# Performance work log

Hardware: AMD Instinct MI355X
Metric: run time of the kernel (lower is better)

## Reference

```python
import jax, jax.numpy as jnp
import numpy as np

IMG = 416                      # image_shape
DIST = 1075.0                  # isocenter_distance
N_ANG = 320                    # 360 / rotation_resolution(=1.125 deg)
N_DET = IMG                    # detector bins
N_SAMP = IMG                   # integration samples per ray
SCALE = 512.0 / 416.0 * 0.03   # self.scale


def _ray_coords():
    """Pixel-space sample coordinates for every (angle, detector, sample).
    Returns cols, rows of shape [N_ANG, N_DET, N_SAMP] and the step length dt."""
    thetas = (jnp.arange(N_ANG, dtype=jnp.float32) * np.float32(2.0 * np.pi / N_ANG))
    half_diag = (IMG / 2.0) * np.sqrt(2.0)
    gamma_max = np.float32(np.arcsin(half_diag / DIST))  # half fan angle covering image
    gammas = jnp.linspace(-gamma_max, gamma_max, N_DET, dtype=jnp.float32)
    ray_len = np.float32(IMG * np.sqrt(2.0))             # chord length through image
    ts = jnp.linspace(np.float32(DIST - ray_len / 2.0),
                      np.float32(DIST + ray_len / 2.0), N_SAMP, dtype=jnp.float32)
    dt = float(ray_len / (N_SAMP - 1))

    th = thetas[:, None, None]        # [A,1,1]
    gm = gammas[None, :, None]        # [1,D,1]
    t = ts[None, None, :]             # [1,1,S]
    # source position on circle of radius DIST, ray direction toward detector
    sx = np.float32(DIST) * jnp.cos(th)
    sy = np.float32(DIST) * jnp.sin(th)
    x = sx - t * jnp.cos(th + gm)     # [A,D,S] world coords (isocenter at origin)
    y = sy - t * jnp.sin(th + gm)
    ctr = np.float32((IMG - 1) / 2.0)
    return x + ctr, y + ctr, dt       # pixel (col, row) coordinates


def _bilinear(img, cols, rows):
    """Zero-padded bilinear sampling of img[H,W] at float (row,col) coords."""
    c0 = jnp.floor(cols)
    r0 = jnp.floor(rows)
    wc = cols - c0
    wr = rows - r0
    c0i = c0.astype(jnp.int32)
    r0i = r0.astype(jnp.int32)

    def g(ri, ci):
        inb = (ri >= 0) & (ri < IMG) & (ci >= 0) & (ci < IMG)
        v = img[jnp.clip(ri, 0, IMG - 1), jnp.clip(ci, 0, IMG - 1)]
        return jnp.where(inb, v, jnp.float32(0.0))

    return (g(r0i, c0i) * (1 - wr) * (1 - wc)
            + g(r0i, c0i + 1) * (1 - wr) * wc
            + g(r0i + 1, c0i) * wr * (1 - wc)
            + g(r0i + 1, c0i + 1) * wr * wc)


def fan_beam_fp(vol):
    """vol: [B,H,W] -> sinogram [B, N_ANG, N_DET] via ray integration."""
    cols, rows, dt = _ray_coords()
    proj_one = lambda img: _bilinear(img, cols, rows).sum(axis=-1) * jnp.float32(dt)
    return jax.vmap(proj_one)(vol)


def setup_inputs() -> dict:
    key = jax.random.key(0)
    k1, k2 = jax.random.split(key)
    inp = jax.random.normal(k1, (1, 1, IMG, IMG), dtype=jnp.float32)
    tgt = jax.random.normal(k2, (1, 1, IMG, IMG), dtype=jnp.float32)
    return {"input": inp, "target": tgt}


def reference(input, target):
    input_proj = fan_beam_fp(input[:, 0])   # squeeze(1)
    target_proj = fan_beam_fp(target[:, 0])
    return jnp.mean((input_proj - target_proj) ** 2) * jnp.float32(SCALE)
```

## Files before the change

kernel.cpp:

```cpp
#include <hip/hip_runtime.h>
#include <math.h>

#define IMG 416
#define N_ANG 320
#define N_DET 416
#define N_SAMP 416

#define GSTRIDE 464
#define GROWS   432
#define GBYTES  ((size_t)GROWS * GSTRIDE)
#define GWORDS  (GROWS * GSTRIDE / 4)

#define SPLANE  (N_ANG * N_DET)
#define SBYTES  ((size_t)4 * SPLANE * sizeof(float))
#define WSNEED  (GBYTES + SBYTES)

#define LROWS   228
#define LSTRIDE 232

typedef float vfloat2 __attribute__((ext_vector_type(2)));

__global__ __launch_bounds__(256) void pack_kernel(const float* __restrict__ a,
                                                   const float* __restrict__ b,
                                                   unsigned int* __restrict__ G,
                                                   float* __restrict__ out) {
    int i = blockIdx.x * 256 + threadIdx.x;
    if (i == 0) out[0] = 0.0f;
    if (i >= GWORDS) return;
    int pr = i / (GSTRIDE / 4);
    int wc = i - pr * (GSTRIDE / 4);
    int r  = pr - 8;
    int c0 = wc * 4 - 8;
    float v[4];
    #pragma unroll
    for (int j = 0; j < 4; ++j) {
        int c = c0 + j;
        float val = 0.0f;
        if ((unsigned)r < (unsigned)IMG && (unsigned)c < (unsigned)IMG) {
            int idx = r * IMG + c;
            val = a[idx] - b[idx];
        }
        v[j] = val;
    }
    unsigned int u = __builtin_amdgcn_cvt_pk_fp8_f32(v[0], v[1], 0u, false);
    u = __builtin_amdgcn_cvt_pk_fp8_f32(v[2], v[3], u, true);
    G[i] = u;
}

__global__ void zero_out_kernel(float* __restrict__ out) {
    if (threadIdx.x == 0) out[0] = 0.0f;
}

__global__ __launch_bounds__(448) void proj_lds(const unsigned int* __restrict__ G,
                                                float* __restrict__ S,
                                                float theta_step, float gmax,
                                                float gstep, float t0,
                                                float dtstep) {
    __shared__ unsigned char L[LROWS * LSTRIDE];

    const int blk = blockIdx.x;
    const int a  = blk >> 2;
    const int q  = blk & 3;
    const int qi = q >> 1, qj = q & 1;
    const int r0 = qi ? 222 : -2;
    const int c0 = qj ? 220 : -4;
    const int nrows = qi ? 197 : 227;

    {
        const int gbase = ((r0 + 8) * GSTRIDE + (c0 + 8)) >> 2;
        const int total = nrows * 58;
        for (int i = threadIdx.x; i < total; i += 448) {
            int rr = i / 58;
            int cc = i - rr * 58;
            unsigned int w = G[gbase + rr * 116 + cc];
            *(unsigned int*)(&L[rr * LSTRIDE + cc * 4]) = w;
        }
    }
    __syncthreads();

    const int d = threadIdx.x;
    if (d < N_DET) {
        const float theta = (float)a * theta_step;
        const float gamma = fmaf((float)d, gstep, -gmax);
        float s1, c1, s2, c2;
        sincosf(theta, &s1, &c1);
        sincosf(theta + gamma, &s2, &c2);
        const float sx = fmaf(1075.0f, c1, 207.5f);
        const float sy = fmaf(1075.0f, s1, 207.5f);

        const float C0 = fmaf(-t0, c2, sx), dc = dtstep * c2;
        const float R0 = fmaf(-t0, s2, sy), dr = dtstep * s2;

        const float cl = qj ? 224.0f : -2.0f, ch = qj ? 418.0f : 224.0f;
        const float rl = qi ? 224.0f : -2.0f, rh = qi ? 418.0f : 224.0f;

        int klo = 0, khi = N_SAMP - 1;
        auto clip1 = [&](float X0, float dX, float lo, float hi) {
            if (fabsf(dX) < 1e-8f) {
                if (!(X0 >= lo && X0 < hi)) { klo = 1; khi = 0; }
            } else {
                float x1 = (X0 - hi) / dX;
                float x2 = (X0 - lo) / dX;
                x1 = fminf(fmaxf(x1, -1e6f), 1e6f);
                x2 = fminf(fmaxf(x2, -1e6f), 1e6f);
                int lo_k, hi_k;
                if (dX > 0.0f) { lo_k = (int)floorf(x1) + 1; hi_k = (int)floorf(x2); }
                else           { lo_k = (int)ceilf(x2);      hi_k = (int)ceilf(x1) - 1; }
                klo = max(klo, lo_k);
                khi = min(khi, hi_k);
            }
        };
        clip1(C0, dc, cl, ch);
        clip1(R0, dr, rl, rh);

        float acc = 0.0f;
        if (klo <= khi) {
            float colR = fmaf(-(float)klo, dc, C0) - (float)c0;
            float rowR = fmaf(-(float)klo, dr, R0) - (float)r0;
            #pragma unroll 4
            for (int k = klo; k <= khi; ++k) {
                const int ci = (int)colR;
                const int ri = (int)rowR;
                const float wc = colR - (float)ci;
                const float wr = rowR - (float)ri;
                const int base = ri * LSTRIDE + ci;
                const unsigned int b00 = L[base];
                const unsigned int b01 = L[base + 1];
                const unsigned int b10 = L[base + LSTRIDE];
                const unsigned int b11 = L[base + LSTRIDE + 1];
                const vfloat2 lo2 = __builtin_amdgcn_cvt_pk_f32_fp8(b00 | (b01 << 8), false);
                const vfloat2 hi2 = __builtin_amdgcn_cvt_pk_f32_fp8(b10 | (b11 << 8), false);
                const float top = fmaf(wc, lo2[1] - lo2[0], lo2[0]);
                const float bot = fmaf(wc, hi2[1] - hi2[0], hi2[0]);
                acc = fmaf(wr, bot - top, acc + top);
                colR -= dc;
                rowR -= dr;
            }
        }
        S[q * SPLANE + a * N_DET + d] = acc;
    }
}

__global__ __launch_bounds__(256) void reduce_kernel(const float* __restrict__ S,
                                                     float* __restrict__ out,
                                                     float coef) {
    const int i = blockIdx.x * 256 + threadIdx.x;
    float v = 0.0f;
    if (i < SPLANE)
        v = (S[i] + S[SPLANE + i]) + (S[2 * SPLANE + i] + S[3 * SPLANE + i]);
    float sq = v * v;
    #pragma unroll
    for (int m = 32; m > 0; m >>= 1) sq += __shfl_down(sq, m, 64);
    __shared__ float w[4];
    const int lane = threadIdx.x & 63;
    if (lane == 0) w[threadIdx.x >> 6] = sq;
    __syncthreads();
    if (threadIdx.x == 0)
        atomicAdd(out, (w[0] + w[1] + w[2] + w[3]) * coef);
}

__global__ __launch_bounds__(256) void proj_fused(const float* __restrict__ imgA,
                                                  const float* __restrict__ imgB,
                                                  float* __restrict__ out,
                                                  float theta_step, float gmax,
                                                  float gstep, float t0,
                                                  float dtstep, float coef) {
    const int idx = blockIdx.x * 256 + threadIdx.x;
    const int a  = idx / N_DET;
    const int dd = idx - a * N_DET;
    const float theta = (float)a * theta_step;
    const float gamma = fmaf((float)dd, gstep, -gmax);
    float s1, c1, s2, c2;
    sincosf(theta, &s1, &c1);
    sincosf(theta + gamma, &s2, &c2);
    const float sx = 1075.0f * c1 + 207.5f;
    const float sy = 1075.0f * s1 + 207.5f;
    float acc = 0.0f;
    #pragma unroll 4
    for (int s = 0; s < N_SAMP; ++s) {
        const float t   = fmaf((float)s, dtstep, t0);
        const float col = fmaf(-t, c2, sx);
        const float row = fmaf(-t, s2, sy);
        const float c0 = floorf(col);
        const float r0 = floorf(row);
        const float wc = col - c0;
        const float wr = row - r0;
        const int ci = (int)c0;
        const int ri = (int)r0;
        auto Gv = [&](int r, int c) -> float {
            if ((unsigned)r < (unsigned)IMG && (unsigned)c < (unsigned)IMG)
                return imgA[r * IMG + c] - imgB[r * IMG + c];
            return 0.0f;
        };
        const float v00 = Gv(ri, ci);
        const float v01 = Gv(ri, ci + 1);
        const float v10 = Gv(ri + 1, ci);
        const float v11 = Gv(ri + 1, ci + 1);
        const float top = fmaf(wc, v01 - v00, v00);
        const float bot = fmaf(wc, v11 - v10, v10);
        acc += fmaf(wr, bot - top, top);
    }
    float sq = acc * acc;
    #pragma unroll
    for (int o = 32; o > 0; o >>= 1) sq += __shfl_down(sq, o, 64);
    __shared__ float wsum[4];
    const int lane = threadIdx.x & 63;
    if (lane == 0) wsum[threadIdx.x >> 6] = sq;
    __syncthreads();
    if (threadIdx.x == 0)
        atomicAdd(out, (wsum[0] + wsum[1] + wsum[2] + wsum[3]) * coef);
}

extern "C" void kernel_launch(void* const* d_in, const int* in_sizes, int n_in,
                              void* d_out, int out_size, void* d_ws, size_t ws_size,
                              hipStream_t stream) {
    const float* in = (const float*)d_in[0];
    const float* tg = (const float*)d_in[1];
    float* out = (float*)d_out;

    const double half_diag = (IMG / 2.0) * sqrt(2.0);
    const double ray_len   = IMG * sqrt(2.0);
    const float  gmax      = (float)asin(half_diag / 1075.0);
    const float  gstep     = (float)(2.0 * (double)gmax / (N_DET - 1));
    const float  t0        = (float)(1075.0 - ray_len / 2.0);
    const float  dtstep    = (float)(ray_len / (N_SAMP - 1));
    const float  theta_step = (float)(2.0 * M_PI / N_ANG);
    const double dt        = ray_len / (N_SAMP - 1);
    const double SCALE     = 512.0 / 416.0 * 0.03;
    const float  coef      = (float)(dt * dt * SCALE / ((double)N_ANG * N_DET));

    if (ws_size >= WSNEED) {
        unsigned int* G = (unsigned int*)d_ws;
        float* S = (float*)((char*)d_ws + GBYTES);
        pack_kernel<<<(GWORDS + 255) / 256, 256, 0, stream>>>(in, tg, G, out);
        proj_lds<<<N_ANG * 4, 448, 0, stream>>>(G, S, theta_step, gmax, gstep,
                                                t0, dtstep);
        reduce_kernel<<<SPLANE / 256, 256, 0, stream>>>(S, out, coef);
    } else {
        zero_out_kernel<<<1, 64, 0, stream>>>(out);
        proj_fused<<<(N_ANG * N_DET) / 256, 256, 0, stream>>>(
            in, tg, out, theta_step, gmax, gstep, t0, dtstep, coef);
    }
}
```

Measured before the change: 105.5 us.

## Pack 2x2 fp8 quads per word, split image into 16 tiles, atomic-accumulate

The packed difference image now stores each pixel's 2x2 bilinear neighbourhood as four fp8 bytes in one 32-bit word, so each sample needs one LDS load instead of four byte loads. The image is split into a 4x4 grid of 104-pixel tiles per angle (16 blocks per angle instead of 4), which shrinks the LDS footprint and raises parallelism; tiles are loaded with 16-byte vector copies. Partial ray sums are combined with atomicAdd into a single sinogram plane zeroed by the pack kernel, removing the 4-plane reduction. This costs 4x global storage for the packed image, more redundant tile loads and more per-block setup per ray, plus float atomics with nondeterministic summation order.

```diff
diff --git a/kernel.cpp b/kernel.cpp
--- a/kernel.cpp
+++ b/kernel.cpp
@@ -6,74 +6,71 @@
 #define N_DET 416
 #define N_SAMP 416
 
-#define GSTRIDE 464
-#define GROWS   432
-#define GBYTES  ((size_t)GROWS * GSTRIDE)
-#define GWORDS  (GROWS * GSTRIDE / 4)
+#define GQSTRIDE 424
+#define GQROWS   420
+#define GQWORDS  (GQROWS * GQSTRIDE)
+#define GQBYTES  ((size_t)GQWORDS * 4)
 
 #define SPLANE  (N_ANG * N_DET)
-#define SBYTES  ((size_t)4 * SPLANE * sizeof(float))
-#define WSNEED  (GBYTES + SBYTES)
-
-#define LROWS   228
-#define LSTRIDE 232
+#define SBYTES  ((size_t)SPLANE * 4)
+#define WSNEED  (GQBYTES + SBYTES)
+
+#define LSTRIDE 116
+#define LWORDS  (108 * LSTRIDE)
 
 typedef float vfloat2 __attribute__((ext_vector_type(2)));
 
 __global__ __launch_bounds__(256) void pack_kernel(const float* __restrict__ a,
                                                    const float* __restrict__ b,
-                                                   unsigned int* __restrict__ G,
+                                                   unsigned int* __restrict__ Gq,
+                                                   float* __restrict__ S,
                                                    float* __restrict__ out) {
     int i = blockIdx.x * 256 + threadIdx.x;
     if (i == 0) out[0] = 0.0f;
-    if (i >= GWORDS) return;
-    int pr = i / (GSTRIDE / 4);
-    int wc = i - pr * (GSTRIDE / 4);
-    int r  = pr - 8;
-    int c0 = wc * 4 - 8;
-    float v[4];
-    #pragma unroll
-    for (int j = 0; j < 4; ++j) {
-        int c = c0 + j;
-        float val = 0.0f;
+    if (i < SPLANE) S[i] = 0.0f;
+    if (i >= GQWORDS) return;
+    int row  = i / GQSTRIDE;
+    int colw = i - row * GQSTRIDE;
+    int pr = row - 2, pc = colw - 2;
+    auto D = [&](int r, int c) -> float {
         if ((unsigned)r < (unsigned)IMG && (unsigned)c < (unsigned)IMG) {
             int idx = r * IMG + c;
-            val = a[idx] - b[idx];
+            return a[idx] - b[idx];
         }
-        v[j] = val;
-    }
-    unsigned int u = __builtin_amdgcn_cvt_pk_fp8_f32(v[0], v[1], 0u, false);
-    u = __builtin_amdgcn_cvt_pk_fp8_f32(v[2], v[3], u, true);
-    G[i] = u;
+        return 0.0f;
+    };
+    const float v00 = D(pr, pc),     v01 = D(pr, pc + 1);
+    const float v10 = D(pr + 1, pc), v11 = D(pr + 1, pc + 1);
+    unsigned int u = __builtin_amdgcn_cvt_pk_fp8_f32(v00, v01, 0u, false);
+    u = __builtin_amdgcn_cvt_pk_fp8_f32(v10, v11, u, true);
+    Gq[i] = u;
 }
 
 __global__ void zero_out_kernel(float* __restrict__ out) {
     if (threadIdx.x == 0) out[0] = 0.0f;
 }
 
-__global__ __launch_bounds__(448) void proj_lds(const unsigned int* __restrict__ G,
+__global__ __launch_bounds__(448) void proj_lds(const unsigned int* __restrict__ Gq,
                                                 float* __restrict__ S,
                                                 float theta_step, float gmax,
                                                 float gstep, float t0,
                                                 float dtstep) {
-    __shared__ unsigned char L[LROWS * LSTRIDE];
-
-    const int blk = blockIdx.x;
-    const int a  = blk >> 2;
-    const int q  = blk & 3;
-    const int qi = q >> 1, qj = q & 1;
-    const int r0 = qi ? 222 : -2;
-    const int c0 = qj ? 220 : -4;
-    const int nrows = qi ? 197 : 227;
+    __shared__ unsigned int Lw[LWORDS];
+
+    const int blk  = blockIdx.x;
+    const int a    = blk >> 4;
+    const int tile = blk & 15;
+    const int qi = tile >> 2, qj = tile & 3;
+    const int r0 = 104 * qi - 2;
+    const int c0 = 104 * qj - 2;
 
     {
-        const int gbase = ((r0 + 8) * GSTRIDE + (c0 + 8)) >> 2;
-        const int total = nrows * 58;
-        for (int i = threadIdx.x; i < total; i += 448) {
-            int rr = i / 58;
-            int cc = i - rr * 58;
-            unsigned int w = G[gbase + rr * 116 + cc];
-            *(unsigned int*)(&L[rr * LSTRIDE + cc * 4]) = w;
+        const uint4* __restrict__ src =
+            (const uint4*)(Gq + (r0 + 2) * GQSTRIDE + (c0 + 2));
+        for (int i = threadIdx.x; i < 108 * 27; i += 448) {
+            int rr = i / 27, cc = i - rr * 27;
+            uint4 w = src[rr * (GQSTRIDE / 4) + cc];
+            *(uint4*)&Lw[rr * LSTRIDE + cc * 4] = w;
         }
     }
     __syncthreads();
@@ -91,16 +88,19 @@
         const float C0 = fmaf(-t0, c2, sx), dc = dtstep * c2;
         const float R0 = fmaf(-t0, s2, sy), dr = dtstep * s2;
 
-        const float cl = qj ? 224.0f : -2.0f, ch = qj ? 418.0f : 224.0f;
-        const float rl = qi ? 224.0f : -2.0f, rh = qi ? 418.0f : 224.0f;
+        const float cl = (qj == 0) ? -1.0f : 104.0f * qj;
+        const float ch = (qj == 3) ? 416.0f : 104.0f * (qj + 1);
+        const float rl = (qi == 0) ? -1.0f : 104.0f * qi;
+        const float rh = (qi == 3) ? 416.0f : 104.0f * (qi + 1);
 
         int klo = 0, khi = N_SAMP - 1;
         auto clip1 = [&](float X0, float dX, float lo, float hi) {
             if (fabsf(dX) < 1e-8f) {
                 if (!(X0 >= lo && X0 < hi)) { klo = 1; khi = 0; }
             } else {
-                float x1 = (X0 - hi) / dX;
-                float x2 = (X0 - lo) / dX;
+                const float inv = 1.0f / dX;
+                float x1 = (X0 - hi) * inv;
+                float x2 = (X0 - lo) * inv;
                 x1 = fminf(fmaxf(x1, -1e6f), 1e6f);
                 x2 = fminf(fmaxf(x2, -1e6f), 1e6f);
                 int lo_k, hi_k;
@@ -113,31 +113,27 @@
         clip1(C0, dc, cl, ch);
         clip1(R0, dr, rl, rh);
 
-        float acc = 0.0f;
         if (klo <= khi) {
             float colR = fmaf(-(float)klo, dc, C0) - (float)c0;
             float rowR = fmaf(-(float)klo, dr, R0) - (float)r0;
+            float acc = 0.0f;
             #pragma unroll 4
             for (int k = klo; k <= khi; ++k) {
                 const int ci = (int)colR;
                 const int ri = (int)rowR;
                 const float wc = colR - (float)ci;
                 const float wr = rowR - (float)ri;
-                const int base = ri * LSTRIDE + ci;
-                const unsigned int b00 = L[base];
-                const unsigned int b01 = L[base + 1];
-                const unsigned int b10 = L[base + LSTRIDE];
-                const unsigned int b11 = L[base + LSTRIDE + 1];
-                const vfloat2 lo2 = __builtin_amdgcn_cvt_pk_f32_fp8(b00 | (b01 << 8), false);
-                const vfloat2 hi2 = __builtin_amdgcn_cvt_pk_f32_fp8(b10 | (b11 << 8), false);
+                const unsigned int u = Lw[ri * LSTRIDE + ci];
+                const vfloat2 lo2 = __builtin_amdgcn_cvt_pk_f32_fp8(u, false);
+                const vfloat2 hi2 = __builtin_amdgcn_cvt_pk_f32_fp8(u, true);
                 const float top = fmaf(wc, lo2[1] - lo2[0], lo2[0]);
                 const float bot = fmaf(wc, hi2[1] - hi2[0], hi2[0]);
                 acc = fmaf(wr, bot - top, acc + top);
                 colR -= dc;
                 rowR -= dr;
             }
+            atomicAdd(&S[a * N_DET + d], acc);
         }
-        S[q * SPLANE + a * N_DET + d] = acc;
     }
 }
 
@@ -145,9 +141,7 @@
                                                      float* __restrict__ out,
                                                      float coef) {
     const int i = blockIdx.x * 256 + threadIdx.x;
-    float v = 0.0f;
-    if (i < SPLANE)
-        v = (S[i] + S[SPLANE + i]) + (S[2 * SPLANE + i] + S[3 * SPLANE + i]);
+    float v = (i < SPLANE) ? S[i] : 0.0f;
     float sq = v * v;
     #pragma unroll
     for (int m = 32; m > 0; m >>= 1) sq += __shfl_down(sq, m, 64);
@@ -230,12 +224,12 @@
     const float  coef      = (float)(dt * dt * SCALE / ((double)N_ANG * N_DET));
 
     if (ws_size >= WSNEED) {
-        unsigned int* G = (unsigned int*)d_ws;
-        float* S = (float*)((char*)d_ws + GBYTES);
-        pack_kernel<<<(GWORDS + 255) / 256, 256, 0, stream>>>(in, tg, G, out);
-        proj_lds<<<N_ANG * 4, 448, 0, stream>>>(G, S, theta_step, gmax, gstep,
-                                                t0, dtstep);
-        reduce_kernel<<<SPLANE / 256, 256, 0, stream>>>(S, out, coef);
+        unsigned int* Gq = (unsigned int*)d_ws;
+        float* S = (float*)((char*)d_ws + GQBYTES);
+        pack_kernel<<<(GQWORDS + 255) / 256, 256, 0, stream>>>(in, tg, Gq, S, out);
+        proj_lds<<<N_ANG * 16, 448, 0, stream>>>(Gq, S, theta_step, gmax, gstep,
+                                                 t0, dtstep);
+        reduce_kernel<<<(SPLANE + 255) / 256, 256, 0, stream>>>(S, out, coef);
     } else {
         zero_out_kernel<<<1, 64, 0, stream>>>(out);
         proj_fused<<<(N_ANG * N_DET) / 256, 256, 0, stream>>>(
```

Result: slower. 124.7 us (+18.2%).
